# Optimization experiments

Hardware: AMD Instinct MI355X
Metric: run time of the kernel (lower is better)

Reference implementation:

```python
import jax, jax.numpy as jnp
import numpy as np

B, T, C, HS, E, NR, P = 2, 2048, 1024, 64, 8, 6, 4
H = C // HS
FF = 4 * C
NT = E - NR


def _ln(x, w, b):
    m = x.mean(-1, keepdims=True)
    v = x.var(-1, keepdims=True)
    return (x - m) * jax.lax.rsqrt(v + 1e-5) * w + b


def _rwkv_scan(r, k, v, w):
    # r,k,v,w: (B,T,H,D); per-head linear-attention recurrence with channel decay
    def step(S, inp):
        r_t, k_t, v_t, w_t = inp  # (B,H,D)
        S = S * w_t[..., :, None] + k_t[..., :, None] * v_t[..., None, :]
        y = jnp.einsum('bhk,bhkv->bhv', r_t, S)
        return S, y
    Bb, Tt, Hh, Dd = r.shape
    S0 = jnp.zeros((Bb, Hh, Dd, Dd), r.dtype)
    xs = tuple(jnp.moveaxis(a, 1, 0) for a in (r, k, v, w))
    _, ys = jax.lax.scan(step, S0, xs)
    return jnp.moveaxis(ys, 0, 1)


def setup_inputs() -> dict:
    key = jax.random.key(0)
    ks = jax.random.split(key, 24)
    s = 1.0 / np.sqrt(C)
    n = lambda k, sh, sc: jax.random.normal(k, sh, jnp.float32) * sc
    return {
        'x': n(ks[0], (B, T, C), 1.0),
        'v_first': jnp.zeros((B, T, C), jnp.float32),
        'capital_shares': jax.random.uniform(ks[1], (E,), dtype=jnp.float32),
        'ln1_w': jnp.ones((C,), jnp.float32), 'ln1_b': jnp.zeros((C,), jnp.float32),
        'ln2_w': jnp.ones((C,), jnp.float32), 'ln2_b': jnp.zeros((C,), jnp.float32),
        'Wr': n(ks[2], (C, C), s), 'Wk': n(ks[3], (C, C), s),
        'Wv': n(ks[4], (C, C), s), 'Ww': n(ks[5], (C, C), s),
        'w_bias': 2.0 * jnp.ones((C,), jnp.float32),
        'Wo': n(ks[6], (C, C), s),
        'conf_w': n(ks[7], (E, C), s), 'conf_b': jnp.zeros((E,), jnp.float32),
        'Wd': n(ks[8], (C, 1), s), 'bd': jnp.zeros((1,), jnp.float32),
        'Wa': n(ks[9], (C, E), s), 'ba': jnp.zeros((E,), jnp.float32),
        'Wb': n(ks[10], (2 * C, P * C), 1.0 / np.sqrt(2 * C)),
        'ffn_Wr': n(ks[11], (NR, C, C), s),
        'ffn_Wk': n(ks[12], (NR, C, FF), s),
        'ffn_Wv': n(ks[13], (NR, FF, C), 1.0 / np.sqrt(FF)),
        'tr_Wq': n(ks[14], (NT, C, C), s), 'tr_Wk': n(ks[15], (NT, C, C), s),
        'tr_Wv': n(ks[16], (NT, C, C), s), 'tr_Wo': n(ks[17], (NT, C, C), s),
    }


def _forward(x, v_first, capital_shares, ln1_w, ln1_b, ln2_w, ln2_b,
             Wr, Wk, Wv, Ww, w_bias, Wo, conf_w, conf_b, Wd, bd, Wa, ba, Wb,
             ffn_Wr, ffn_Wk, ffn_Wv, tr_Wq, tr_Wk, tr_Wv, tr_Wo):
    # --- attention stage: ln1 -> RWKV7 TimeMix -> residual -> ln2 ---
    x_ln = _ln(x, ln1_w, ln1_b)
    r = (x_ln @ Wr).reshape(B, T, H, HS)
    k = (x_ln @ Wk).reshape(B, T, H, HS)
    v_flat = x_ln @ Wv
    v = v_flat.reshape(B, T, H, HS)
    w = jax.nn.sigmoid(x_ln @ Ww + w_bias).reshape(B, T, H, HS)  # decay in (0,1)
    rwkv_state = _rwkv_scan(r, k, v, w).reshape(B, T, C)
    att_out = rwkv_state @ Wo
    x_after_att = x + att_out
    h = _ln(x_after_att, ln2_w, ln2_b)
    # --- no-grad market routing: confidences + critic + top-2 auction ---
    rh = jax.lax.stop_gradient(h)
    conf = jax.nn.sigmoid(jnp.einsum('btc,ec->bte', rh, conf_w) + conf_b)  # (B,T,E)
    difficulty = jax.nn.softplus(rh @ Wd + bd)          # (B,T,1)
    affinity = rh @ Wa + ba                             # (B,T,E)
    subsidy = jax.nn.softmax(affinity, axis=-1)         # critic subsidy
    bids = conf * capital_shares + subsidy
    top_vals, winners = jax.lax.top_k(bids, 2)          # (B,T,2)
    weights = jax.lax.stop_gradient(jax.nn.softmax(top_vals, axis=-1))
    # --- bridge prefix for transformer experts ---
    BT = B * T
    flat_h = h.reshape(BT, C)
    flat_state = rwkv_state.reshape(BT, C)
    prefix = jnp.tanh(jnp.concatenate([flat_h, flat_state], -1) @ Wb).reshape(BT, P, C)
    # --- top-2 expert mixing: gate==0 for unselected tokens (same math as masked dispatch) ---
    final_out = jnp.zeros_like(h)
    scale = 1.0 / np.sqrt(HS)
    for e in range(E):
        gate = (weights * (winners == e)).sum(-1)  # (B,T)
        if e < NR:  # sparse RWKV FFN expert: relu^2 channel-mix with receptance gate
            kk = jax.nn.relu(h @ ffn_Wk[e]) ** 2
            out_e = jax.nn.sigmoid(h @ ffn_Wr[e]) * (kk @ ffn_Wv[e])
        else:       # linear transformer expert: cross-attend token over its bridge prefix
            t = e - NR
            q = (flat_h @ tr_Wq[t]).reshape(BT, H, HS)
            kp = (prefix @ tr_Wk[t]).reshape(BT, P, H, HS)
            vp = (prefix @ tr_Wv[t]).reshape(BT, P, H, HS)
            a = jax.nn.softmax(jnp.einsum('nhd,nphd->nhp', q, kp) * scale, -1)
            out_e = (jnp.einsum('nhp,nphd->nhd', a, vp).reshape(BT, C) @ tr_Wo[t]).reshape(B, T, C)
        final_out = final_out + gate[..., None] * out_e
    x_out = x_after_att + final_out
    return x_out, v_flat  # layer 0: v_first is set to the value projection


def reference(x, v_first, capital_shares, ln1_w, ln1_b, ln2_w, ln2_b,
              Wr, Wk, Wv, Ww, w_bias, Wo, conf_w, conf_b, Wd, bd, Wa, ba, Wb,
              ffn_Wr, ffn_Wk, ffn_Wv, tr_Wq, tr_Wk, tr_Wv, tr_Wo):
    return _forward(x, v_first, capital_shares, ln1_w, ln1_b, ln2_w, ln2_b,
                    Wr, Wk, Wv, Ww, w_bias, Wo, conf_w, conf_b, Wd, bd, Wa, ba, Wb,
                    ffn_Wr, ffn_Wk, ffn_Wv, tr_Wq, tr_Wk, tr_Wv, tr_Wo)
```

## Files before the change

kernel.cpp:

```cpp
#include <hip/hip_runtime.h>
#include <hip/hip_bf16.h>
#include <math.h>

#define Bn   2
#define Tn   2048
#define Cdim 1024
#define HSn  64
#define En   8
#define NRn  6
#define Pn   4
#define Hn   16
#define FFn  4096
#define NTn  2
#define BTn  4096
#define CHL  128
#define NCH  16

typedef __attribute__((ext_vector_type(8))) short bfrag;
typedef __attribute__((ext_vector_type(4))) float f32x4;

__device__ __forceinline__ void gl_lds16(const void* g, void* l) {
    __builtin_amdgcn_global_load_lds(
        (const __attribute__((address_space(1))) unsigned int*)g,
        (__attribute__((address_space(3))) unsigned int*)l, 16, 0, 0);
}

__device__ __forceinline__ float sigm(float v) { return 1.f / (1.f + expf(-v)); }

__global__ __launch_bounds__(256) void ln_kernel(const float* __restrict__ x,
                                                 const float* __restrict__ w,
                                                 const float* __restrict__ b,
                                                 float* __restrict__ out_f,
                                                 __hip_bfloat16* __restrict__ out_hi,
                                                 __hip_bfloat16* __restrict__ out_lo) {
    int row = blockIdx.x;
    const float* xr = x + (size_t)row * Cdim;
    float s = 0.f, s2 = 0.f;
    for (int c = threadIdx.x; c < Cdim; c += 256) {
        float v = xr[c];
        s += v; s2 += v * v;
    }
    __shared__ float rs[256], rs2[256];
    rs[threadIdx.x] = s; rs2[threadIdx.x] = s2;
    __syncthreads();
    for (int st = 128; st > 0; st >>= 1) {
        if (threadIdx.x < st) {
            rs[threadIdx.x]  += rs[threadIdx.x + st];
            rs2[threadIdx.x] += rs2[threadIdx.x + st];
        }
        __syncthreads();
    }
    float mean = rs[0] / Cdim;
    float var  = rs2[0] / Cdim - mean * mean;
    float inv  = rsqrtf(var + 1e-5f);
    for (int c = threadIdx.x; c < Cdim; c += 256) {
        float v = (xr[c] - mean) * inv * w[c] + b[c];
        size_t idx = (size_t)row * Cdim + c;
        if (out_f) out_f[idx] = v;
        if (out_hi) {
            __hip_bfloat16 hi = __float2bfloat16(v);
            out_hi[idx] = hi;
            if (out_lo) out_lo[idx] = __float2bfloat16(v - __bfloat162float(hi));
        }
    }
}

__global__ __launch_bounds__(256) void convT_kernel(const float* __restrict__ W,
                                                    __hip_bfloat16* __restrict__ Wt,
                                                    int K, int N) {
    __shared__ float tile[32][33];
    int k0 = blockIdx.y * 32, n0 = blockIdx.x * 32;
    int tx = threadIdx.x, ty = threadIdx.y;
#pragma unroll
    for (int i = 0; i < 32; i += 8)
        tile[ty + i][tx] = W[(size_t)(k0 + ty + i) * N + n0 + tx];
    __syncthreads();
#pragma unroll
    for (int i = 0; i < 32; i += 8)
        Wt[(size_t)(n0 + ty + i) * K + k0 + tx] = __float2bfloat16(tile[tx][ty + i]);
}

__global__ __launch_bounds__(256) void convT_split_kernel(const float* __restrict__ W,
                                                          __hip_bfloat16* __restrict__ Wh,
                                                          __hip_bfloat16* __restrict__ Wl,
                                                          int K, int N) {
    __shared__ float tile[32][33];
    int k0 = blockIdx.y * 32, n0 = blockIdx.x * 32;
    int tx = threadIdx.x, ty = threadIdx.y;
#pragma unroll
    for (int i = 0; i < 32; i += 8)
        tile[ty + i][tx] = W[(size_t)(k0 + ty + i) * N + n0 + tx];
    __syncthreads();
#pragma unroll
    for (int i = 0; i < 32; i += 8) {
        float v = tile[tx][ty + i];
        __hip_bfloat16 hi = __float2bfloat16(v);
        size_t o = (size_t)(n0 + ty + i) * K + k0 + tx;
        Wh[o] = hi;
        Wl[o] = __float2bfloat16(v - __bfloat162float(hi));
    }
}

__global__ __launch_bounds__(256) void convT_split4_kernel(
    const float* __restrict__ W0, const float* __restrict__ W1,
    const float* __restrict__ W2, const float* __restrict__ W3,
    __hip_bfloat16* __restrict__ Wh, __hip_bfloat16* __restrict__ Wl) {
    int z = blockIdx.z;
    const float* W = (z == 0) ? W0 : (z == 1) ? W1 : (z == 2) ? W2 : W3;
    __hip_bfloat16* Whz = Wh + (size_t)z * Cdim * Cdim;
    __hip_bfloat16* Wlz = Wl + (size_t)z * Cdim * Cdim;
    __shared__ float tile[32][33];
    int k0 = blockIdx.y * 32, n0 = blockIdx.x * 32;
    int tx = threadIdx.x, ty = threadIdx.y;
#pragma unroll
    for (int i = 0; i < 32; i += 8)
        tile[ty + i][tx] = W[(size_t)(k0 + ty + i) * Cdim + n0 + tx];
    __syncthreads();
#pragma unroll
    for (int i = 0; i < 32; i += 8) {
        float v = tile[tx][ty + i];
        __hip_bfloat16 hi = __float2bfloat16(v);
        size_t o = (size_t)(n0 + ty + i) * Cdim + k0 + tx;
        Whz[o] = hi;
        Wlz[o] = __float2bfloat16(v - __bfloat162float(hi));
    }
}

__global__ __launch_bounds__(256) void convT_ffn_kernel(
    const float* __restrict__ Wr, const float* __restrict__ Wk,
    const float* __restrict__ Wv, __hip_bfloat16* __restrict__ dRK,
    __hip_bfloat16* __restrict__ dV) {
    int z = blockIdx.z;
    const float* src; __hip_bfloat16* dst; int srcLD, dstLD;
    if (z == 0) {
        src = Wr; dst = dRK; srcLD = 1024; dstLD = 1024;
    } else if (z < 5) {
        int s = z - 1;
        src = Wk + (size_t)s * 1024;
        dst = dRK + (size_t)(1024 + s * 1024) * 1024;
        srcLD = FFn; dstLD = 1024;
    } else {
        int s = z - 5;
        src = Wv + (size_t)s * 1024 * Cdim;
        dst = dV + (size_t)s * 1024;
        srcLD = Cdim; dstLD = FFn;
    }
    __shared__ float tile[32][33];
    int k0 = blockIdx.y * 32, n0 = blockIdx.x * 32;
    int tx = threadIdx.x, ty = threadIdx.y;
#pragma unroll
    for (int i = 0; i < 32; i += 8)
        tile[ty + i][tx] = src[(size_t)(k0 + ty + i) * srcLD + n0 + tx];
    __syncthreads();
#pragma unroll
    for (int i = 0; i < 32; i += 8)
        dst[(size_t)(n0 + ty + i) * dstLD + k0 + tx] = __float2bfloat16(tile[tx][ty + i]);
}

__global__ __launch_bounds__(256) void convT_tr_kernel(
    const float* __restrict__ W0, const float* __restrict__ W1,
    const float* __restrict__ W2, const float* __restrict__ W3,
    __hip_bfloat16* __restrict__ dst) {
    int z = blockIdx.z;
    const float* W = (z == 0) ? W0 : (z == 1) ? W1 : (z == 2) ? W2 : W3;
    __hip_bfloat16* Wt = dst + (size_t)z * Cdim * Cdim;
    __shared__ float tile[32][33];
    int k0 = blockIdx.y * 32, n0 = blockIdx.x * 32;
    int tx = threadIdx.x, ty = threadIdx.y;
#pragma unroll
    for (int i = 0; i < 32; i += 8)
        tile[ty + i][tx] = W[(size_t)(k0 + ty + i) * Cdim + n0 + tx];
    __syncthreads();
#pragma unroll
    for (int i = 0; i < 32; i += 8)
        Wt[(size_t)(n0 + ty + i) * Cdim + k0 + tx] = __float2bfloat16(tile[tx][ty + i]);
}

enum { EP3_QKVW = 0, EP3_ADD = 1 };

template <int EP>
__global__ __launch_bounds__(256) void bgemm3_kernel(
    const __hip_bfloat16* __restrict__ Ah, const __hip_bfloat16* __restrict__ Al,
    const __hip_bfloat16* __restrict__ Bh, const __hip_bfloat16* __restrict__ Bl,
    float* __restrict__ o0, float* __restrict__ o1,
    float* __restrict__ o2, float* __restrict__ o3,
    int M, int N, int K, const float* __restrict__ aux) {
    __shared__ __align__(16) __hip_bfloat16 Ahs[4096], Als[4096], Bhs[4096], Bls[4096];
    int tid = threadIdx.x;
    int m0 = blockIdx.y * 128, n0 = blockIdx.x * 128;
    int l = tid & 63, wv = tid >> 6;
    int wm = (wv >> 1) * 64, wn = (wv & 1) * 64;
    int lr = l & 15, lq = l >> 4;

    f32x4 acc[4][4];
#pragma unroll
    for (int i = 0; i < 4; i++)
#pragma unroll
        for (int j = 0; j < 4; j++) acc[i][j] = (f32x4){0.f, 0.f, 0.f, 0.f};

    int srow = tid >> 2;
    int sq = (tid & 3) ^ (srow & 3);
    size_t arow = (size_t)(m0 + srow) * K + (sq << 3);
    size_t brow = (size_t)(n0 + srow) * K + (sq << 3);

    for (int kt = 0; kt < K; kt += 32) {
#pragma unroll
        for (int r = 0; r < 2; r++) {
            size_t go = (size_t)(r * 64) * K + kt;
            int lo = r * 2048 + tid * 8;
            gl_lds16(Ah + arow + go, Ahs + lo);
            gl_lds16(Al + arow + go, Als + lo);
            gl_lds16(Bh + brow + go, Bhs + lo);
            gl_lds16(Bl + brow + go, Bls + lo);
        }
        __syncthreads();
        bfrag ah[4], al[4], bh[4], bl[4];
#pragma unroll
        for (int mi = 0; mi < 4; mi++) {
            int rr = wm + mi * 16 + lr;
            int off = rr * 32 + ((lq ^ (rr & 3)) << 3);
            ah[mi] = *(const bfrag*)&Ahs[off];
            al[mi] = *(const bfrag*)&Als[off];
        }
#pragma unroll
        for (int ni = 0; ni < 4; ni++) {
            int rr = wn + ni * 16 + lr;
            int off = rr * 32 + ((lq ^ (rr & 3)) << 3);
            bh[ni] = *(const bfrag*)&Bhs[off];
            bl[ni] = *(const bfrag*)&Bls[off];
        }
#pragma unroll
        for (int mi = 0; mi < 4; mi++)
#pragma unroll
            for (int ni = 0; ni < 4; ni++) {
                acc[mi][ni] = __builtin_amdgcn_mfma_f32_16x16x32_bf16(ah[mi], bh[ni], acc[mi][ni], 0, 0, 0);
                acc[mi][ni] = __builtin_amdgcn_mfma_f32_16x16x32_bf16(al[mi], bh[ni], acc[mi][ni], 0, 0, 0);
                acc[mi][ni] = __builtin_amdgcn_mfma_f32_16x16x32_bf16(ah[mi], bl[ni], acc[mi][ni], 0, 0, 0);
            }
        __syncthreads();
    }

#pragma unroll
    for (int mi = 0; mi < 4; mi++) {
#pragma unroll
        for (int r = 0; r < 4; r++) {
            int row = m0 + wm + mi * 16 + lq * 4 + r;
#pragma unroll
            for (int ni = 0; ni < 4; ni++) {
                int col = n0 + wn + ni * 16 + lr;
                float v = acc[mi][ni][r];
                if (EP == EP3_QKVW) {
                    int sel = col >> 10, cc = col & 1023;
                    size_t idx = (size_t)row * 1024 + cc;
                    if (sel == 0) o0[idx] = v;
                    else if (sel == 1) o1[idx] = v;
                    else if (sel == 2) o2[idx] = v;
                    else o3[idx] = sigm(v + aux[cc]);
                } else {
                    size_t idx = (size_t)row * N + col;
                    o0[idx] = aux[idx] + v;
                }
            }
        }
    }
}

enum { EP_TANHB = 0, EP_BF16 = 1, EP_MOE = 2, EP_MOEM = 3, EP_FFN1 = 4, EP_KV = 5 };

template <int EP>
__global__ __launch_bounds__(256) void bgemm_kernel(
    const __hip_bfloat16* __restrict__ A, const __hip_bfloat16* __restrict__ Bt,
    void* __restrict__ Cv, void* __restrict__ Cv2, int M, int N, int K,
    const int* __restrict__ meta, int e,
    const int* __restrict__ tokidx, const float* __restrict__ tokgate,
    const float* __restrict__ aux2) {
    int rows = M;
    int offA = 0;
    const int* sidx = nullptr;
    const float* sgate = nullptr;
    if (meta) {
        if (EP == EP_TANHB) {
            rows = meta[6] + meta[7];
        } else if (EP == EP_KV) {
            rows = meta[e] * 4;
            offA = (meta[8 + e] - meta[14]) * 4;
        } else {
            rows = meta[e];
            if (EP == EP_MOE || EP == EP_MOEM) {
                sidx = tokidx + meta[8 + e];
                sgate = tokgate + meta[8 + e];
            } else {
                offA = meta[8 + e];
            }
        }
    }
    int m0 = blockIdx.y * 128;
    if (m0 >= rows) return;

    __shared__ __align__(16) __hip_bfloat16 Asm[8192];
    __shared__ __align__(16) __hip_bfloat16 Bsm[8192];
    int tid = threadIdx.x;
    int n0 = blockIdx.x * 128;
    int l = tid & 63, wv = tid >> 6;
    int wm = (wv >> 1) * 64, wn = (wv & 1) * 64;
    int lr = l & 15, lq = l >> 4;

    f32x4 acc[4][4];
#pragma unroll
    for (int i = 0; i < 4; i++)
#pragma unroll
        for (int j = 0; j < 4; j++) acc[i][j] = (f32x4){0.f, 0.f, 0.f, 0.f};

    int srow = tid >> 3;
    int sq = (tid & 7) ^ (srow & 7);
    size_t arow = (size_t)(m0 + offA + srow) * K + (sq << 3);
    size_t brow = (size_t)(n0 + srow) * K + (sq << 3);

    int ks = K / gridDim.z;
    int kbeg = blockIdx.z * ks, kend = kbeg + ks;

    for (int kt = kbeg; kt < kend; kt += 64) {
#pragma unroll
        for (int c = 0; c < 4; c++) {
            size_t go = (size_t)(c * 32) * K + kt;
            gl_lds16(A + arow + go, Asm + c * 2048 + tid * 8);
            gl_lds16(Bt + brow + go, Bsm + c * 2048 + tid * 8);
        }
        __syncthreads();
#pragma unroll
        for (int kc = 0; kc < 64; kc += 32) {
            bfrag af[4], bf[4];
#pragma unroll
            for (int mi = 0; mi < 4; mi++) {
                int rr = wm + mi * 16 + lr;
                af[mi] = *(const bfrag*)&Asm[rr * 64 + ((((kc >> 3) + lq) ^ (rr & 7)) << 3)];
            }
#pragma unroll
            for (int ni = 0; ni < 4; ni++) {
                int rr = wn + ni * 16 + lr;
                bf[ni] = *(const bfrag*)&Bsm[rr * 64 + ((((kc >> 3) + lq) ^ (rr & 7)) << 3)];
            }
#pragma unroll
            for (int mi = 0; mi < 4; mi++)
#pragma unroll
                for (int ni = 0; ni < 4; ni++)
                    acc[mi][ni] = __builtin_amdgcn_mfma_f32_16x16x32_bf16(
                        af[mi], bf[ni], acc[mi][ni], 0, 0, 0);
        }
        __syncthreads();
    }

    float* Cf = (float*)Cv;
    __hip_bfloat16* Cb = (__hip_bfloat16*)Cv;
#pragma unroll
    for (int mi = 0; mi < 4; mi++) {
#pragma unroll
        for (int r = 0; r < 4; r++) {
            int row = m0 + wm + mi * 16 + lq * 4 + r;
            if (row >= rows) continue;
            int t = 0; float g = 0.f;
            if (EP == EP_MOE || EP == EP_MOEM) { t = sidx[row]; g = sgate[row]; }
#pragma unroll
            for (int ni = 0; ni < 4; ni++) {
                int col = n0 + wn + ni * 16 + lr;
                float v = acc[mi][ni][r];
                if (EP == EP_TANHB) {
                    Cb[(size_t)row * N + col] = __float2bfloat16(tanhf(v));
                } else if (EP == EP_BF16) {
                    Cb[(size_t)row * N + col] = __float2bfloat16(v);
                } else if (EP == EP_MOE) {
                    float* p = Cf + (size_t)t * 1024 + col;
                    *p = *p + g * v;
                } else if (EP == EP_MOEM) {
                    atomicAdd(Cf + (size_t)t * 1024 + col,
                              g * aux2[(size_t)row * 1024 + col] * v);
                } else if (EP == EP_FFN1) {
                    if ((col >> 10) == 0) {
                        Cf[(size_t)row * 1024 + col] = sigm(v);
                    } else {
                        float q = fmaxf(v, 0.f);
                        ((__hip_bfloat16*)Cv2)[(size_t)row * 4096 + col - 1024] =
                            __float2bfloat16(q * q);
                    }
                } else if (EP == EP_KV) {
                    if ((col >> 10) == 0)
                        Cb[(size_t)row * 1024 + col] = __float2bfloat16(v);
                    else
                        ((__hip_bfloat16*)Cv2)[(size_t)row * 1024 + col - 1024] =
                            __float2bfloat16(v);
                }
            }
        }
    }
}

__global__ __launch_bounds__(256) void scan_pass1(
    const float* __restrict__ k, const float* __restrict__ v,
    const float* __restrict__ w, float* __restrict__ Mbuf,
    float* __restrict__ Pbuf) {
    int c = blockIdx.x, bh = blockIdx.y;
    int b = bh >> 4, h = bh & 15;
    int tid = threadIdx.x, j = tid & 63, ig = tid >> 6;
    __shared__ float sbuf[2][3][64];
    float S[16], P[16];
#pragma unroll
    for (int ii = 0; ii < 16; ii++) { S[ii] = 0.f; P[ii] = 1.f; }

    size_t base = ((size_t)b * Tn + (size_t)c * CHL) * Cdim + (size_t)h * HSn + j;
    const float* srcs[3] = {k, v, w};
    const float* myp = (ig > 0) ? srcs[ig - 1] + base : k + base;

    const int CH = 8;
    float buf[CH];
#pragma unroll
    for (int u = 0; u < CH; u++) buf[u] = (ig > 0) ? myp[(size_t)u * Cdim] : 0.f;

    for (int tc = 0; tc < CHL; tc += CH) {
        float nbuf[CH];
#pragma unroll
        for (int u = 0; u < CH; u++) {
            int t2 = tc + CH + u;
            nbuf[u] = (ig > 0 && t2 < CHL) ? myp[(size_t)t2 * Cdim] : 0.f;
        }
#pragma unroll
        for (int u = 0; u < CH; u++) {
            int p = (tc + u) & 1;
            if (ig > 0) sbuf[p][ig - 1][j] = buf[u];
            __syncthreads();
            float vj = sbuf[p][1][j];
            const float* skp = sbuf[p][0];
            const float* swp = sbuf[p][2];
#pragma unroll
            for (int ii = 0; ii < 16; ii++) {
                int i = (ig << 4) + ii;
                float wi = swp[i];
                S[ii] = S[ii] * wi + skp[i] * vj;
                P[ii] *= wi;
            }
        }
#pragma unroll
        for (int u = 0; u < CH; u++) buf[u] = nbuf[u];
    }
    size_t mo = ((size_t)c * 32 + bh) * 4096;
#pragma unroll
    for (int ii = 0; ii < 16; ii++)
        Mbuf[mo + (size_t)((ig << 4) + ii) * 64 + j] = S[ii];
    if (j == 0) {
#pragma unroll
        for (int ii = 0; ii < 16; ii++)
            Pbuf[((size_t)c * 32 + bh) * 64 + (ig << 4) + ii] = P[ii];
    }
}

__global__ __launch_bounds__(256) void scan_pass2(
    const float* __restrict__ Mbuf, const float* __restrict__ Pbuf,
    float* __restrict__ Sinb) {
    int bh = blockIdx.y;
    int idx = blockIdx.x * 256 + threadIdx.x;
    int i = idx >> 6;
    float S = 0.f;
    for (int c = 0; c < NCH; c++) {
        size_t o = ((size_t)c * 32 + bh);
        Sinb[o * 4096 + idx] = S;
        S = Pbuf[o * 64 + i] * S + Mbuf[o * 4096 + idx];
    }
}

__global__ __launch_bounds__(256) void scan_pass3(
    const float* __restrict__ r, const float* __restrict__ k,
    const float* __restrict__ v, const float* __restrict__ w,
    const float* __restrict__ Sinb,
    __hip_bfloat16* __restrict__ sh, __hip_bfloat16* __restrict__ sl) {
    int c = blockIdx.x, bh = blockIdx.y;
    int b = bh >> 4, h = bh & 15;
    int tid = threadIdx.x, j = tid & 63, ig = tid >> 6;
    __shared__ float sbuf[2][4][64];
    __shared__ float red[2][4][64];
    float S[16];
    size_t so = ((size_t)c * 32 + bh) * 4096;
#pragma unroll
    for (int ii = 0; ii < 16; ii++)
        S[ii] = Sinb[so + (size_t)((ig << 4) + ii) * 64 + j];

    size_t base = ((size_t)b * Tn + (size_t)c * CHL) * Cdim + (size_t)h * HSn + j;
    const float* srcs[4] = {r, k, v, w};
    const float* myp = srcs[ig] + base;

    const int CH = 8;
    float buf[CH];
#pragma unroll
    for (int u = 0; u < CH; u++) buf[u] = myp[(size_t)u * Cdim];
    float part_prev = 0.f;

    for (int tc = 0; tc < CHL; tc += CH) {
        float nbuf[CH];
#pragma unroll
        for (int u = 0; u < CH; u++) {
            int t2 = tc + CH + u;
            nbuf[u] = (t2 < CHL) ? myp[(size_t)t2 * Cdim] : 0.f;
        }
#pragma unroll
        for (int u = 0; u < CH; u++) {
            int t = tc + u;
            int p = t & 1;
            sbuf[p][ig][j] = buf[u];
            red[p][ig][j] = part_prev;
            __syncthreads();
            if (ig == 0 && t > 0) {
                float val = red[p][0][j] + red[p][1][j] + red[p][2][j] + red[p][3][j];
                __hip_bfloat16 hi = __float2bfloat16(val);
                size_t pos = base + (size_t)(t - 1) * Cdim;
                sh[pos] = hi;
                sl[pos] = __float2bfloat16(val - __bfloat162float(hi));
            }
            float vj = sbuf[p][2][j];
            const float* srp = sbuf[p][0];
            const float* skp = sbuf[p][1];
            const float* swp = sbuf[p][3];
            float part = 0.f;
#pragma unroll
            for (int ii = 0; ii < 16; ii++) {
                int i = (ig << 4) + ii;
                S[ii] = S[ii] * swp[i] + skp[i] * vj;
                part += srp[i] * S[ii];
            }
            part_prev = part;
        }
#pragma unroll
        for (int u = 0; u < CH; u++) buf[u] = nbuf[u];
    }
    red[0][ig][j] = part_prev;
    __syncthreads();
    if (ig == 0) {
        float val = red[0][0][j] + red[0][1][j] + red[0][2][j] + red[0][3][j];
        __hip_bfloat16 hi = __float2bfloat16(val);
        size_t pos = base + (size_t)(CHL - 1) * Cdim;
        sh[pos] = hi;
        sl[pos] = __float2bfloat16(val - __bfloat162float(hi));
    }
}

__global__ __launch_bounds__(256) void routing_kernel(
    const float* __restrict__ h, const float* __restrict__ conf_w,
    const float* __restrict__ conf_b, const float* __restrict__ Wa,
    const float* __restrict__ ba, const float* __restrict__ cap,
    int* __restrict__ meta, int2* __restrict__ winfo, float2* __restrict__ gvals) {
    int row = blockIdx.x;
    const float* hr = h + (size_t)row * Cdim;
    float pc[8], pa[8];
#pragma unroll
    for (int e = 0; e < 8; e++) { pc[e] = 0.f; pa[e] = 0.f; }
    for (int c = threadIdx.x; c < Cdim; c += 256) {
        float hv = hr[c];
#pragma unroll
        for (int e = 0; e < 8; e++) {
            pc[e] += hv * conf_w[(size_t)e * Cdim + c];
            pa[e] += hv * Wa[(size_t)c * En + e];
        }
    }
    __shared__ float red[256];
    __shared__ float vals[16];
    for (int e = 0; e < 16; e++) {
        red[threadIdx.x] = (e < 8) ? pc[e] : pa[e - 8];
        __syncthreads();
        for (int st = 128; st > 0; st >>= 1) {
            if (threadIdx.x < st) red[threadIdx.x] += red[threadIdx.x + st];
            __syncthreads();
        }
        if (threadIdx.x == 0) vals[e] = red[0];
        __syncthreads();
    }
    if (threadIdx.x == 0) {
        float conf[8], aff[8];
        for (int e = 0; e < 8; e++) {
            conf[e] = sigm(vals[e] + conf_b[e]);
            aff[e]  = vals[8 + e] + ba[e];
        }
        float mx = aff[0];
        for (int e = 1; e < 8; e++) mx = fmaxf(mx, aff[e]);
        float se = 0.f, ex[8];
        for (int e = 0; e < 8; e++) { ex[e] = expf(aff[e] - mx); se += ex[e]; }
        float bids[8];
        for (int e = 0; e < 8; e++) bids[e] = conf[e] * cap[e] + ex[e] / se;
        int w0 = 0;
        for (int e = 1; e < 8; e++) if (bids[e] > bids[w0]) w0 = e;
        int w1 = -1;
        for (int e = 0; e < 8; e++) {
            if (e == w0) continue;
            if (w1 < 0 || bids[e] > bids[w1]) w1 = e;
        }
        float e1 = expf(bids[w1] - bids[w0]);
        float g0 = 1.f / (1.f + e1);
        float g1 = e1 / (1.f + e1);
        winfo[row] = make_int2(w0, w1);
        gvals[row] = make_float2(g0, g1);
        atomicAdd(&meta[w0], 1);
        atomicAdd(&meta[w1], 1);
    }
}

__global__ void offsets_kernel(int* __restrict__ meta) {
    if (threadIdx.x == 0 && blockIdx.x == 0) {
        int acc = 0;
        for (int e = 0; e < 8; e++) { meta[8 + e] = acc; acc += meta[e]; }
    }
}

__global__ __launch_bounds__(256) void assign_kernel(
    const int2* __restrict__ winfo, const float2* __restrict__ gvals,
    const int* __restrict__ meta, int* __restrict__ tokidx,
    float* __restrict__ tokgate, int2* __restrict__ posbuf) {
    int e = blockIdx.x;
    int tid = threadIdx.x;
    __shared__ int scn[256];
    int base = meta[8 + e];
    for (int c = 0; c < BTn; c += 256) {
        int t = c + tid;
        int2 w = winfo[t];
        int m0 = (w.x == e) ? 1 : 0;
        int m1 = (w.y == e) ? 1 : 0;
        int cnt = m0 + m1;
        scn[tid] = cnt;
        __syncthreads();
        for (int st = 1; st < 256; st <<= 1) {
            int vv = (tid >= st) ? scn[tid - st] : 0;
            __syncthreads();
            scn[tid] += vv;
            __syncthreads();
        }
        int excl = scn[tid] - cnt;
        int tot = scn[255];
        if (m0) {
            int p = base + excl;
            tokidx[p] = t; tokgate[p] = gvals[t].x; posbuf[t].x = p;
        }
        if (m1) {
            int p = base + excl;
            tokidx[p] = t; tokgate[p] = gvals[t].y; posbuf[t].y = p;
        }
        base += tot;
        __syncthreads();
    }
}

__global__ __launch_bounds__(256) void gather_kernel(
    const __hip_bfloat16* __restrict__ h_bf, const __hip_bfloat16* __restrict__ st,
    const int2* __restrict__ winfo, const int2* __restrict__ posbuf,
    const int* __restrict__ meta,
    __hip_bfloat16* __restrict__ hc, __hip_bfloat16* __restrict__ hsc) {
    int t = blockIdx.x;
    int tid = threadIdx.x;
    int2 w = winfo[t];
    int2 p = posbuf[t];
    int off6 = meta[14];
    ushort4 hv = ((const ushort4*)(h_bf + (size_t)t * 1024))[tid];
    ((ushort4*)(hc + (size_t)p.x * 1024))[tid] = hv;
    ((ushort4*)(hc + (size_t)p.y * 1024))[tid] = hv;
    if (w.x >= 6) {
        int lp = p.x - off6;
        ((ushort4*)(hsc + (size_t)lp * 2048))[tid] = hv;
        ((ushort4*)(hsc + (size_t)lp * 2048 + 1024))[tid] =
            ((const ushort4*)(st + (size_t)t * 1024))[tid];
    }
    if (w.y >= 6) {
        int lp = p.y - off6;
        ((ushort4*)(hsc + (size_t)lp * 2048))[tid] = hv;
        ((ushort4*)(hsc + (size_t)lp * 2048 + 1024))[tid] =
            ((const ushort4*)(st + (size_t)t * 1024))[tid];
    }
}

__global__ __launch_bounds__(256) void tr_attn_kernel(
    const __hip_bfloat16* __restrict__ qc, const __hip_bfloat16* __restrict__ kpc,
    const __hip_bfloat16* __restrict__ vpc, __hip_bfloat16* __restrict__ attnc,
    const int* __restrict__ meta, int e) {
    int cnt = meta[e];
    int idx = blockIdx.x * 4 + (threadIdx.x >> 6);
    int lane = threadIdx.x & 63;
    int n = idx >> 4, h = idx & 15;
    if (n >= cnt) return;
    float qd = __bfloat162float(qc[(size_t)n * Cdim + (size_t)h * HSn + lane]);
    float s[4];
#pragma unroll
    for (int p = 0; p < 4; p++) {
        float t = qd * __bfloat162float(kpc[((size_t)n * Pn + p) * Cdim + (size_t)h * HSn + lane]);
        for (int off = 32; off > 0; off >>= 1) t += __shfl_down(t, off);
        s[p] = __shfl(t, 0);
    }
    const float scale = 0.125f;
    float mx = fmaxf(fmaxf(s[0], s[1]), fmaxf(s[2], s[3])) * scale;
    float es = 0.f, a[4];
#pragma unroll
    for (int p = 0; p < 4; p++) { a[p] = expf(s[p] * scale - mx); es += a[p]; }
    float o = 0.f;
#pragma unroll
    for (int p = 0; p < 4; p++)
        o += (a[p] / es) * __bfloat162float(vpc[((size_t)n * Pn + p) * Cdim + (size_t)h * HSn + lane]);
    attnc[(size_t)n * Cdim + (size_t)h * HSn + lane] = __float2bfloat16(o);
}

extern "C" void kernel_launch(void* const* d_in, const int* in_sizes, int n_in,
                              void* d_out, int out_size, void* d_ws, size_t ws_size,
                              hipStream_t stream) {
    const float* x      = (const float*)d_in[0];
    const float* cap    = (const float*)d_in[2];
    const float* ln1_w  = (const float*)d_in[3];
    const float* ln1_b  = (const float*)d_in[4];
    const float* ln2_w  = (const float*)d_in[5];
    const float* ln2_b  = (const float*)d_in[6];
    const float* Wr     = (const float*)d_in[7];
    const float* Wk     = (const float*)d_in[8];
    const float* Wv     = (const float*)d_in[9];
    const float* Ww     = (const float*)d_in[10];
    const float* w_bias = (const float*)d_in[11];
    const float* Wo     = (const float*)d_in[12];
    const float* conf_w = (const float*)d_in[13];
    const float* conf_b = (const float*)d_in[14];
    const float* Wa     = (const float*)d_in[17];
    const float* ba     = (const float*)d_in[18];
    const float* Wb     = (const float*)d_in[19];
    const float* ffn_Wr = (const float*)d_in[20];
    const float* ffn_Wk = (const float*)d_in[21];
    const float* ffn_Wv = (const float*)d_in[22];
    const float* tr_Wq  = (const float*)d_in[23];
    const float* tr_Wk  = (const float*)d_in[24];
    const float* tr_Wv  = (const float*)d_in[25];
    const float* tr_Wo  = (const float*)d_in[26];

    float* xout  = (float*)d_out;
    float* vflat = (float*)d_out + (size_t)BTn * Cdim;

    char* ws = (char*)d_ws;
    const size_t MB = 1ull << 20;
    __hip_bfloat16* xln_hi  = (__hip_bfloat16*)(ws + 0 * MB);
    __hip_bfloat16* xln_lo  = (__hip_bfloat16*)(ws + 8 * MB);
    __hip_bfloat16* Wall_hi = (__hip_bfloat16*)(ws + 16 * MB);
    __hip_bfloat16* Wall_lo = (__hip_bfloat16*)(ws + 24 * MB);
    float*          rbuf    = (float*)(ws + 32 * MB);
    float*          kbuf    = (float*)(ws + 48 * MB);
    float*          wbuf    = (float*)(ws + 64 * MB);
    float*          Pbuf    = (float*)(ws + 80 * MB);
    __hip_bfloat16* Wo_hi   = (__hip_bfloat16*)(ws + 81 * MB);
    __hip_bfloat16* Wo_lo   = (__hip_bfloat16*)(ws + 83 * MB);
    float*          Mbuf    = (float*)(ws + 0 * MB);
    float*          Sinb    = (float*)(ws + 8 * MB);
    __hip_bfloat16* st_hi   = (__hip_bfloat16*)(ws + 16 * MB);
    __hip_bfloat16* st_lo   = (__hip_bfloat16*)(ws + 24 * MB);
    float*          hbuf    = (float*)(ws + 32 * MB);
    __hip_bfloat16* h_bf    = (__hip_bfloat16*)(ws + 48 * MB);
    __hip_bfloat16* hc      = (__hip_bfloat16*)(ws + 56 * MB);
    __hip_bfloat16* hsc     = (__hip_bfloat16*)(ws + 74 * MB);
    __hip_bfloat16* Wt_b    = (__hip_bfloat16*)(ws + 108 * MB);
    __hip_bfloat16* prefixc = (__hip_bfloat16*)(ws + 124 * MB);
    __hip_bfloat16* eWall   = (__hip_bfloat16*)(ws + 0 * MB);
    __hip_bfloat16* eWv_t   = (__hip_bfloat16*)(ws + 10 * MB);
    float*          rg      = (float*)(ws + 18 * MB);
    __hip_bfloat16* kk      = (__hip_bfloat16*)(ws + 74 * MB);
    __hip_bfloat16* vpc     = (__hip_bfloat16*)(ws + 0 * MB);
    __hip_bfloat16* tkv     = (__hip_bfloat16*)(ws + 34 * MB);
    __hip_bfloat16* tq      = (__hip_bfloat16*)(ws + 38 * MB);
    __hip_bfloat16* to_     = (__hip_bfloat16*)(ws + 40 * MB);
    __hip_bfloat16* qc      = (__hip_bfloat16*)(ws + 42 * MB);
    __hip_bfloat16* attnc   = (__hip_bfloat16*)(ws + 74 * MB);
    __hip_bfloat16* kpc     = (__hip_bfloat16*)(ws + 83 * MB);
    int*    meta    = (int*)(ws + 200 * MB);
    int*    tokidx  = (int*)(ws + 200 * MB + (64 << 10));
    float*  tokgate = (float*)(ws + 200 * MB + (128 << 10));
    int2*   winfo   = (int2*)(ws + 200 * MB + (192 << 10));
    float2* gvals   = (float2*)(ws + 200 * MB + (256 << 10));
    int2*   posbuf  = (int2*)(ws + 200 * MB + (320 << 10));
    (void)ws_size; (void)in_sizes; (void)n_in; (void)out_size;

    dim3 blk(256);
    dim3 tblk(32, 8);
    auto grid  = [](int M, int N) { return dim3(N / 128, M / 128); };
    auto tgrid = [](int K, int N) { return dim3(N / 32, K / 32); };
    const size_t CC = (size_t)Cdim * Cdim;

    hipMemsetAsync(meta, 0, 96, stream);
    convT_split4_kernel<<<dim3(32, 32, 4), tblk, 0, stream>>>(Wr, Wk, Wv, Ww, Wall_hi, Wall_lo);
    convT_split_kernel<<<tgrid(Cdim, Cdim), tblk, 0, stream>>>(Wo, Wo_hi, Wo_lo, Cdim, Cdim);
    convT_kernel<<<tgrid(2 * Cdim, Pn * Cdim), tblk, 0, stream>>>(Wb, Wt_b, 2 * Cdim, Pn * Cdim);

    ln_kernel<<<BTn, blk, 0, stream>>>(x, ln1_w, ln1_b, nullptr, xln_hi, xln_lo);
    bgemm3_kernel<EP3_QKVW><<<grid(BTn, 4 * Cdim), blk, 0, stream>>>(
        xln_hi, xln_lo, Wall_hi, Wall_lo, rbuf, kbuf, vflat, wbuf, BTn, 4 * Cdim, Cdim, w_bias);
    scan_pass1<<<dim3(NCH, 32), blk, 0, stream>>>(kbuf, vflat, wbuf, Mbuf, Pbuf);
    scan_pass2<<<dim3(16, 32), blk, 0, stream>>>(Mbuf, Pbuf, Sinb);
    scan_pass3<<<dim3(NCH, 32), blk, 0, stream>>>(rbuf, kbuf, vflat, wbuf, Sinb, st_hi, st_lo);
    bgemm3_kernel<EP3_ADD><<<grid(BTn, Cdim), blk, 0, stream>>>(
        st_hi, st_lo, Wo_hi, Wo_lo, xout, nullptr, nullptr, nullptr, BTn, Cdim, Cdim, x);
    ln_kernel<<<BTn, blk, 0, stream>>>(xout, ln2_w, ln2_b, hbuf, h_bf, nullptr);
    routing_kernel<<<BTn, blk, 0, stream>>>(hbuf, conf_w, conf_b, Wa, ba, cap, meta, winfo, gvals);
    offsets_kernel<<<1, 64, 0, stream>>>(meta);
    assign_kernel<<<dim3(8), blk, 0, stream>>>(winfo, gvals, meta, tokidx, tokgate, posbuf);
    gather_kernel<<<BTn, blk, 0, stream>>>(h_bf, st_hi, winfo, posbuf, meta, hc, hsc);
    bgemm_kernel<EP_TANHB><<<grid(2 * BTn, Pn * Cdim), blk, 0, stream>>>(
        hsc, Wt_b, prefixc, nullptr, 2 * BTn, Pn * Cdim, 2 * Cdim, meta, 0, nullptr, nullptr, nullptr);
    for (int e = 0; e < NRn; e++) {
        convT_ffn_kernel<<<dim3(32, 32, 9), tblk, 0, stream>>>(
            ffn_Wr + (size_t)e * CC, ffn_Wk + (size_t)e * Cdim * FFn,
            ffn_Wv + (size_t)e * FFn * Cdim, eWall, eWv_t);
        bgemm_kernel<EP_FFN1><<<grid(BTn, 5 * Cdim), blk, 0, stream>>>(
            hc, eWall, rg, kk, BTn, 5 * Cdim, Cdim, meta, e, nullptr, nullptr, nullptr);
        bgemm_kernel<EP_MOEM><<<dim3(Cdim / 128, BTn / 128, 2), blk, 0, stream>>>(
            kk, eWv_t, xout, nullptr, BTn, Cdim, FFn, meta, e, tokidx, tokgate, rg);
    }
    for (int t = 0; t < NTn; t++) {
        int e = NRn + t;
        convT_tr_kernel<<<dim3(32, 32, 4), tblk, 0, stream>>>(
            tr_Wk + (size_t)t * CC, tr_Wv + (size_t)t * CC,
            tr_Wq + (size_t)t * CC, tr_Wo + (size_t)t * CC, tkv);
        bgemm_kernel<EP_KV><<<grid(4 * BTn, 2 * Cdim), blk, 0, stream>>>(
            prefixc, tkv, kpc, vpc, 4 * BTn, 2 * Cdim, Cdim, meta, e, nullptr, nullptr, nullptr);
        bgemm_kernel<EP_BF16><<<grid(BTn, Cdim), blk, 0, stream>>>(
            hc, tq, qc, nullptr, BTn, Cdim, Cdim, meta, e, nullptr, nullptr, nullptr);
        tr_attn_kernel<<<(BTn * Hn) / 4, blk, 0, stream>>>(qc, kpc, vpc, attnc, meta, e);
        bgemm_kernel<EP_MOE><<<grid(BTn, Cdim), blk, 0, stream>>>(
            attnc, to_, xout, nullptr, BTn, Cdim, Cdim, meta, e, tokidx, tokgate, nullptr);
    }
}
```

Measured before the change: 1.760 ms.

## Fuse LN2 with routing, batch transformer experts, deepen bgemm3 K-tile

Merges the second layernorm with the routing kernel and removes the offsets kernel by computing expert prefix offsets inside assign_kernel. The two transformer experts' weight conversions, KV projections, Q projections and attention are each batched into a single launch using blockIdx.z. The split-bf16 bgemm3 kernel now loads 64-wide K tiles with an 8-way swizzle, which halves the barrier count and doubles its LDS use. The aim is to cut launch count, intermediate fp32 traffic and sync overhead, at the cost of more LDS per block and more workspace reshuffling.

```diff
diff --git a/kernel.cpp b/kernel.cpp
--- a/kernel.cpp
+++ b/kernel.cpp
@@ -62,6 +62,86 @@
             out_hi[idx] = hi;
             if (out_lo) out_lo[idx] = __float2bfloat16(v - __bfloat162float(hi));
         }
+    }
+}
+
+__global__ __launch_bounds__(256) void ln2_routing_kernel(
+    const float* __restrict__ x, const float* __restrict__ w,
+    const float* __restrict__ b, __hip_bfloat16* __restrict__ out_hi,
+    const float* __restrict__ conf_w, const float* __restrict__ conf_b,
+    const float* __restrict__ Wa, const float* __restrict__ ba,
+    const float* __restrict__ cap, int* __restrict__ meta,
+    int2* __restrict__ winfo, float2* __restrict__ gvals) {
+    int row = blockIdx.x;
+    const float* xr = x + (size_t)row * Cdim;
+    float s = 0.f, s2 = 0.f;
+    for (int c = threadIdx.x; c < Cdim; c += 256) {
+        float v = xr[c];
+        s += v; s2 += v * v;
+    }
+    __shared__ float rs[256], rs2[256];
+    rs[threadIdx.x] = s; rs2[threadIdx.x] = s2;
+    __syncthreads();
+    for (int st = 128; st > 0; st >>= 1) {
+        if (threadIdx.x < st) {
+            rs[threadIdx.x]  += rs[threadIdx.x + st];
+            rs2[threadIdx.x] += rs2[threadIdx.x + st];
+        }
+        __syncthreads();
+    }
+    float mean = rs[0] / Cdim;
+    float var  = rs2[0] / Cdim - mean * mean;
+    float inv  = rsqrtf(var + 1e-5f);
+    float pc[8], pa[8];
+#pragma unroll
+    for (int e = 0; e < 8; e++) { pc[e] = 0.f; pa[e] = 0.f; }
+    for (int c = threadIdx.x; c < Cdim; c += 256) {
+        float hv = (xr[c] - mean) * inv * w[c] + b[c];
+        out_hi[(size_t)row * Cdim + c] = __float2bfloat16(hv);
+#pragma unroll
+        for (int e = 0; e < 8; e++) {
+            pc[e] += hv * conf_w[(size_t)e * Cdim + c];
+            pa[e] += hv * Wa[(size_t)c * En + e];
+        }
+    }
+    __shared__ float red[256];
+    __shared__ float vals[16];
+    for (int e = 0; e < 16; e++) {
+        red[threadIdx.x] = (e < 8) ? pc[e] : pa[e - 8];
+        __syncthreads();
+        for (int st = 128; st > 0; st >>= 1) {
+            if (threadIdx.x < st) red[threadIdx.x] += red[threadIdx.x + st];
+            __syncthreads();
+        }
+        if (threadIdx.x == 0) vals[e] = red[0];
+        __syncthreads();
+    }
+    if (threadIdx.x == 0) {
+        float conf[8], aff[8];
+        for (int e = 0; e < 8; e++) {
+            conf[e] = sigm(vals[e] + conf_b[e]);
+            aff[e]  = vals[8 + e] + ba[e];
+        }
+        float mx = aff[0];
+        for (int e = 1; e < 8; e++) mx = fmaxf(mx, aff[e]);
+        float se = 0.f, ex[8];
+        for (int e = 0; e < 8; e++) { ex[e] = expf(aff[e] - mx); se += ex[e]; }
+        float bids[8];
+        for (int e = 0; e < 8; e++) bids[e] = conf[e] * cap[e] + ex[e] / se;
+        int w0 = 0;
+        for (int e = 1; e < 8; e++) if (bids[e] > bids[w0]) w0 = e;
+        int w1 = -1;
+        for (int e = 0; e < 8; e++) {
+            if (e == w0) continue;
+            if (w1 < 0 || bids[e] > bids[w1]) w1 = e;
+        }
+        float e1 = expf(bids[w1] - bids[w0]);
+        float g0 = 1.f / (1.f + e1);
+        float g1 = e1 / (1.f + e1);
+        winfo[row] = make_int2(w0, w1);
+        gvals[row] = make_float2(g0, g1);
+        atomicAdd(&meta[w0], 1);
+        atomicAdd(&meta[w1], 1);
     }
 }
 
@@ -157,12 +237,14 @@
         dst[(size_t)(n0 + ty + i) * dstLD + k0 + tx] = __float2bfloat16(tile[tx][ty + i]);
 }
 
-__global__ __launch_bounds__(256) void convT_tr_kernel(
-    const float* __restrict__ W0, const float* __restrict__ W1,
-    const float* __restrict__ W2, const float* __restrict__ W3,
+__global__ __launch_bounds__(256) void convT_tr8_kernel(
+    const float* __restrict__ Wk, const float* __restrict__ Wv,
+    const float* __restrict__ Wq, const float* __restrict__ Wo,
     __hip_bfloat16* __restrict__ dst) {
     int z = blockIdx.z;
-    const float* W = (z == 0) ? W0 : (z == 1) ? W1 : (z == 2) ? W2 : W3;
+    int t = z >> 2, j = z & 3;
+    const float* srcs[4] = {Wk, Wv, Wq, Wo};
+    const float* W = srcs[j] + (size_t)t * Cdim * Cdim;
     __hip_bfloat16* Wt = dst + (size_t)z * Cdim * Cdim;
     __shared__ float tile[32][33];
     int k0 = blockIdx.y * 32, n0 = blockIdx.x * 32;
@@ -175,6 +257,7 @@
     for (int i = 0; i < 32; i += 8)
         Wt[(size_t)(n0 + ty + i) * Cdim + k0 + tx] = __float2bfloat16(tile[tx][ty + i]);
 }
+
 
 enum { EP3_QKVW = 0, EP3_ADD = 1 };
 
@@ -185,7 +268,7 @@
     float* __restrict__ o0, float* __restrict__ o1,
     float* __restrict__ o2, float* __restrict__ o3,
     int M, int N, int K, const float* __restrict__ aux) {
-    __shared__ __align__(16) __hip_bfloat16 Ahs[4096], Als[4096], Bhs[4096], Bls[4096];
+    __shared__ __align__(16) __hip_bfloat16 Ahs[8192], Als[8192], Bhs[8192], Bls[8192];
     int tid = threadIdx.x;
     int m0 = blockIdx.y * 128, n0 = blockIdx.x * 128;
     int l = tid & 63, wv = tid >> 6;
@@ -198,45 +281,47 @@
 #pragma unroll
         for (int j = 0; j < 4; j++) acc[i][j] = (f32x4){0.f, 0.f, 0.f, 0.f};
 
-    int srow = tid >> 2;
-    int sq = (tid & 3) ^ (srow & 3);
+    int srow = tid >> 3;
+    int sq = (tid & 7) ^ (srow & 7);
     size_t arow = (size_t)(m0 + srow) * K + (sq << 3);
     size_t brow = (size_t)(n0 + srow) * K + (sq << 3);
 
-    for (int kt = 0; kt < K; kt += 32) {
-#pragma unroll
-        for (int r = 0; r < 2; r++) {
-            size_t go = (size_t)(r * 64) * K + kt;
-            int lo = r * 2048 + tid * 8;
-            gl_lds16(Ah + arow + go, Ahs + lo);
-            gl_lds16(Al + arow + go, Als + lo);
-            gl_lds16(Bh + brow + go, Bhs + lo);
-            gl_lds16(Bl + brow + go, Bls + lo);
-        }
-        __syncthreads();
-        bfrag ah[4], al[4], bh[4], bl[4];
-#pragma unroll
-        for (int mi = 0; mi < 4; mi++) {
-            int rr = wm + mi * 16 + lr;
-            int off = rr * 32 + ((lq ^ (rr & 3)) << 3);
-            ah[mi] = *(const bfrag*)&Ahs[off];
-            al[mi] = *(const bfrag*)&Als[off];
-        }
-#pragma unroll
-        for (int ni = 0; ni < 4; ni++) {
-            int rr = wn + ni * 16 + lr;
-            int off = rr * 32 + ((lq ^ (rr & 3)) << 3);
-            bh[ni] = *(const bfrag*)&Bhs[off];
-            bl[ni] = *(const bfrag*)&Bls[off];
-        }
-#pragma unroll
-        for (int mi = 0; mi < 4; mi++)
+    for (int kt = 0; kt < K; kt += 64) {
+#pragma unroll
+        for (int c = 0; c < 4; c++) {
+            size_t go = (size_t)(c * 32) * K + kt;
+            gl_lds16(Ah + arow + go, Ahs + c * 2048 + tid * 8);
+            gl_lds16(Al + arow + go, Als + c * 2048 + tid * 8);
+            gl_lds16(Bh + brow + go, Bhs + c * 2048 + tid * 8);
+            gl_lds16(Bl + brow + go, Bls + c * 2048 + tid * 8);
+        }
+        __syncthreads();
+#pragma unroll
+        for (int kc = 0; kc < 64; kc += 32) {
+            bfrag ah[4], al[4], bh[4], bl[4];
+#pragma unroll
+            for (int mi = 0; mi < 4; mi++) {
+                int rr = wm + mi * 16 + lr;
+                int off = rr * 64 + ((((kc >> 3) + lq) ^ (rr & 7)) << 3);
+                ah[mi] = *(const bfrag*)&Ahs[off];
+                al[mi] = *(const bfrag*)&Als[off];
+            }
 #pragma unroll
             for (int ni = 0; ni < 4; ni++) {
-                acc[mi][ni] = __builtin_amdgcn_mfma_f32_16x16x32_bf16(ah[mi], bh[ni], acc[mi][ni], 0, 0, 0);
-                acc[mi][ni] = __builtin_amdgcn_mfma_f32_16x16x32_bf16(al[mi], bh[ni], acc[mi][ni], 0, 0, 0);
-                acc[mi][ni] = __builtin_amdgcn_mfma_f32_16x16x32_bf16(ah[mi], bl[ni], acc[mi][ni], 0, 0, 0);
+                int rr = wn + ni * 16 + lr;
+                int off = rr * 64 + ((((kc >> 3) + lq) ^ (rr & 7)) << 3);
+                bh[ni] = *(const bfrag*)&Bhs[off];
+                bl[ni] = *(const bfrag*)&Bls[off];
             }
+#pragma unroll
+            for (int mi = 0; mi < 4; mi++)
+#pragma unroll
+                for (int ni = 0; ni < 4; ni++) {
+                    acc[mi][ni] = __builtin_amdgcn_mfma_f32_16x16x32_bf16(ah[mi], bh[ni], acc[mi][ni], 0, 0, 0);
+                    acc[mi][ni] = __builtin_amdgcn_mfma_f32_16x16x32_bf16(al[mi], bh[ni], acc[mi][ni], 0, 0, 0);
+                    acc[mi][ni] = __builtin_amdgcn_mfma_f32_16x16x32_bf16(ah[mi], bl[ni], acc[mi][ni], 0, 0, 0);
+                }
+        }
         __syncthreads();
     }
 
@@ -265,7 +350,7 @@
     }
 }
 
-enum { EP_TANHB = 0, EP_BF16 = 1, EP_MOE = 2, EP_MOEM = 3, EP_FFN1 = 4, EP_KV = 5 };
+enum { EP_TANHB = 0, EP_Q = 1, EP_MOE = 2, EP_MOEM = 3, EP_FFN1 = 4, EP_KV = 5 };
 
 template <int EP>
 __global__ __launch_bounds__(256) void bgemm_kernel(
@@ -274,24 +359,40 @@
     const int* __restrict__ meta, int e,
     const int* __restrict__ tokidx, const float* __restrict__ tokgate,
     const float* __restrict__ aux2) {
+    const size_t CC_ = (size_t)Cdim * Cdim;
     int rows = M;
     int offA = 0;
+    int outoff = 0;
+    const __hip_bfloat16* Bp = Bt;
     const int* sidx = nullptr;
     const float* sgate = nullptr;
     if (meta) {
         if (EP == EP_TANHB) {
             rows = meta[6] + meta[7];
         } else if (EP == EP_KV) {
-            rows = meta[e] * 4;
-            offA = (meta[8 + e] - meta[14]) * 4;
+            int zx = blockIdx.z;
+            rows = meta[6 + zx] * 4;
+            offA = (meta[8 + 6 + zx] - meta[14]) * 4;
+            outoff = offA;
+            Bp = Bt + (size_t)(zx * 4) * CC_;
+        } else if (EP == EP_Q) {
+            int zx = blockIdx.z;
+            rows = meta[6 + zx];
+            offA = meta[8 + 6 + zx];
+            outoff = meta[8 + 6 + zx] - meta[14];
+            Bp = Bt + (size_t)(zx * 4 + 2) * CC_;
+        } else if (EP == EP_MOE) {
+            rows = meta[e];
+            offA = meta[8 + e] - meta[14];
+            sidx = tokidx + meta[8 + e];
+            sgate = tokgate + meta[8 + e];
+        } else if (EP == EP_MOEM) {
+            rows = meta[e];
+            sidx = tokidx + meta[8 + e];
+            sgate = tokgate + meta[8 + e];
         } else {
             rows = meta[e];
-            if (EP == EP_MOE || EP == EP_MOEM) {
-                sidx = tokidx + meta[8 + e];
-                sgate = tokgate + meta[8 + e];
-            } else {
-                offA = meta[8 + e];
-            }
+            offA = meta[8 + e];
         }
     }
     int m0 = blockIdx.y * 128;
@@ -316,15 +417,20 @@
     size_t arow = (size_t)(m0 + offA + srow) * K + (sq << 3);
     size_t brow = (size_t)(n0 + srow) * K + (sq << 3);
 
-    int ks = K / gridDim.z;
-    int kbeg = blockIdx.z * ks, kend = kbeg + ks;
+    int kbeg, kend;
+    if (EP == EP_KV || EP == EP_Q) {
+        kbeg = 0; kend = K;
+    } else {
+        int ks = K / gridDim.z;
+        kbeg = blockIdx.z * ks; kend = kbeg + ks;
+    }
 
     for (int kt = kbeg; kt < kend; kt += 64) {
 #pragma unroll
         for (int c = 0; c < 4; c++) {
             size_t go = (size_t)(c * 32) * K + kt;
             gl_lds16(A + arow + go, Asm + c * 2048 + tid * 8);
-            gl_lds16(Bt + brow + go, Bsm + c * 2048 + tid * 8);
+            gl_lds16(Bp + brow + go, Bsm + c * 2048 + tid * 8);
         }
         __syncthreads();
 #pragma unroll
@@ -358,6 +464,7 @@
         for (int r = 0; r < 4; r++) {
             int row = m0 + wm + mi * 16 + lq * 4 + r;
             if (row >= rows) continue;
+            int orow = row + outoff;
             int t = 0; float g = 0.f;
             if (EP == EP_MOE || EP == EP_MOEM) { t = sidx[row]; g = sgate[row]; }
 #pragma unroll
@@ -366,8 +473,8 @@
                 float v = acc[mi][ni][r];
                 if (EP == EP_TANHB) {
                     Cb[(size_t)row * N + col] = __float2bfloat16(tanhf(v));
-                } else if (EP == EP_BF16) {
-                    Cb[(size_t)row * N + col] = __float2bfloat16(v);
+                } else if (EP == EP_Q) {
+                    Cb[(size_t)orow * N + col] = __float2bfloat16(v);
                 } else if (EP == EP_MOE) {
                     float* p = Cf + (size_t)t * 1024 + col;
                     *p = *p + g * v;
@@ -384,9 +491,9 @@
                     }
                 } else if (EP == EP_KV) {
                     if ((col >> 10) == 0)
-                        Cb[(size_t)row * 1024 + col] = __float2bfloat16(v);
+                        Cb[(size_t)orow * 1024 + col] = __float2bfloat16(v);
                     else
-                        ((__hip_bfloat16*)Cv2)[(size_t)row * 1024 + col - 1024] =
+                        ((__hip_bfloat16*)Cv2)[(size_t)orow * 1024 + col - 1024] =
                             __float2bfloat16(v);
                 }
             }
@@ -540,80 +647,16 @@
     }
 }
 
-__global__ __launch_bounds__(256) void routing_kernel(
-    const float* __restrict__ h, const float* __restrict__ conf_w,
-    const float* __restrict__ conf_b, const float* __restrict__ Wa,
-    const float* __restrict__ ba, const float* __restrict__ cap,
-    int* __restrict__ meta, int2* __restrict__ winfo, float2* __restrict__ gvals) {
-    int row = blockIdx.x;
-    const float* hr = h + (size_t)row * Cdim;
-    float pc[8], pa[8];
-#pragma unroll
-    for (int e = 0; e < 8; e++) { pc[e] = 0.f; pa[e] = 0.f; }
-    for (int c = threadIdx.x; c < Cdim; c += 256) {
-        float hv = hr[c];
-#pragma unroll
-        for (int e = 0; e < 8; e++) {
-            pc[e] += hv * conf_w[(size_t)e * Cdim + c];
-            pa[e] += hv * Wa[(size_t)c * En + e];
-        }
-    }
-    __shared__ float red[256];
-    __shared__ float vals[16];
-    for (int e = 0; e < 16; e++) {
-        red[threadIdx.x] = (e < 8) ? pc[e] : pa[e - 8];
-        __syncthreads();
-        for (int st = 128; st > 0; st >>= 1) {
-            if (threadIdx.x < st) red[threadIdx.x] += red[threadIdx.x + st];
-            __syncthreads();
-        }
-        if (threadIdx.x == 0) vals[e] = red[0];
-        __syncthreads();
-    }
-    if (threadIdx.x == 0) {
-        float conf[8], aff[8];
-        for (int e = 0; e < 8; e++) {
-            conf[e] = sigm(vals[e] + conf_b[e]);
-            aff[e]  = vals[8 + e] + ba[e];
-        }
-        float mx = aff[0];
-        for (int e = 1; e < 8; e++) mx = fmaxf(mx, aff[e]);
-        float se = 0.f, ex[8];
-        for (int e = 0; e < 8; e++) { ex[e] = expf(aff[e] - mx); se += ex[e]; }
-        float bids[8];
-        for (int e = 0; e < 8; e++) bids[e] = conf[e] * cap[e] + ex[e] / se;
-        int w0 = 0;
-        for (int e = 1; e < 8; e++) if (bids[e] > bids[w0]) w0 = e;
-        int w1 = -1;
-        for (int e = 0; e < 8; e++) {
-            if (e == w0) continue;
-            if (w1 < 0 || bids[e] > bids[w1]) w1 = e;
-        }
-        float e1 = expf(bids[w1] - bids[w0]);
-        float g0 = 1.f / (1.f + e1);
-        float g1 = e1 / (1.f + e1);
-        winfo[row] = make_int2(w0, w1);
-        gvals[row] = make_float2(g0, g1);
-        atomicAdd(&meta[w0], 1);
-        atomicAdd(&meta[w1], 1);
-    }
-}
-
-__global__ void offsets_kernel(int* __restrict__ meta) {
-    if (threadIdx.x == 0 && blockIdx.x == 0) {
-        int acc = 0;
-        for (int e = 0; e < 8; e++) { meta[8 + e] = acc; acc += meta[e]; }
-    }
-}
-
 __global__ __launch_bounds__(256) void assign_kernel(
     const int2* __restrict__ winfo, const float2* __restrict__ gvals,
-    const int* __restrict__ meta, int* __restrict__ tokidx,
+    int* __restrict__ meta, int* __restrict__ tokidx,
     float* __restrict__ tokgate, int2* __restrict__ posbuf) {
     int e = blockIdx.x;
     int tid = threadIdx.x;
     __shared__ int scn[256];
-    int base = meta[8 + e];
+    int base = 0;
+    for (int e2 = 0; e2 < e; ++e2) base += meta[e2];
+    if (tid == 0) meta[8 + e] = base;
     for (int c = 0; c < BTn; c += 256) {
         int t = c + tid;
         int2 w = winfo[t];
@@ -673,8 +716,8 @@
 __global__ __launch_bounds__(256) void tr_attn_kernel(
     const __hip_bfloat16* __restrict__ qc, const __hip_bfloat16* __restrict__ kpc,
     const __hip_bfloat16* __restrict__ vpc, __hip_bfloat16* __restrict__ attnc,
-    const int* __restrict__ meta, int e) {
-    int cnt = meta[e];
+    const int* __restrict__ meta) {
+    int cnt = meta[6] + meta[7];
     int idx = blockIdx.x * 4 + (threadIdx.x >> 6);
     int lane = threadIdx.x & 63;
     int n = idx >> 4, h = idx & 15;
@@ -746,7 +789,6 @@
     float*          Sinb    = (float*)(ws + 8 * MB);
     __hip_bfloat16* st_hi   = (__hip_bfloat16*)(ws + 16 * MB);
     __hip_bfloat16* st_lo   = (__hip_bfloat16*)(ws + 24 * MB);
-    float*          hbuf    = (float*)(ws + 32 * MB);
     __hip_bfloat16* h_bf    = (__hip_bfloat16*)(ws + 48 * MB);
     __hip_bfloat16* hc      = (__hip_bfloat16*)(ws + 56 * MB);
     __hip_bfloat16* hsc     = (__hip_bfloat16*)(ws + 74 * MB);
@@ -758,11 +800,9 @@
     __hip_bfloat16* kk      = (__hip_bfloat16*)(ws + 74 * MB);
     __hip_bfloat16* vpc     = (__hip_bfloat16*)(ws + 0 * MB);
     __hip_bfloat16* tkv     = (__hip_bfloat16*)(ws + 34 * MB);
-    __hip_bfloat16* tq      = (__hip_bfloat16*)(ws + 38 * MB);
-    __hip_bfloat16* to_     = (__hip_bfloat16*)(ws + 40 * MB);
-    __hip_bfloat16* qc      = (__hip_bfloat16*)(ws + 42 * MB);
-    __hip_bfloat16* attnc   = (__hip_bfloat16*)(ws + 74 * MB);
-    __hip_bfloat16* kpc     = (__hip_bfloat16*)(ws + 83 * MB);
+    __hip_bfloat16* kpc     = (__hip_bfloat16*)(ws + 74 * MB);
+    __hip_bfloat16* qc      = (__hip_bfloat16*)(ws + 108 * MB);
+    __hip_bfloat16* attnc   = (__hip_bfloat16*)(ws + 192 * MB);
     int*    meta    = (int*)(ws + 200 * MB);
     int*    tokidx  = (int*)(ws + 200 * MB + (64 << 10));
     float*  tokgate = (float*)(ws + 200 * MB + (128 << 10));
@@ -790,9 +830,8 @@
     scan_pass3<<<dim3(NCH, 32), blk, 0, stream>>>(rbuf, kbuf, vflat, wbuf, Sinb, st_hi, st_lo);
     bgemm3_kernel<EP3_ADD><<<grid(BTn, Cdim), blk, 0, stream>>>(
         st_hi, st_lo, Wo_hi, Wo_lo, xout, nullptr, nullptr, nullptr, BTn, Cdim, Cdim, x);
-    ln_kernel<<<BTn, blk, 0, stream>>>(xout, ln2_w, ln2_b, hbuf, h_bf, nullptr);
-    routing_kernel<<<BTn, blk, 0, stream>>>(hbuf, conf_w, conf_b, Wa, ba, cap, meta, winfo, gvals);
-    offsets_kernel<<<1, 64, 0, stream>>>(meta);
+    ln2_routing_kernel<<<BTn, blk, 0, stream>>>(
+        xout, ln2_w, ln2_b, h_bf, conf_w, conf_b, Wa, ba, cap, meta, winfo, gvals);
     assign_kernel<<<dim3(8), blk, 0, stream>>>(winfo, gvals, meta, tokidx, tokgate, posbuf);
     gather_kernel<<<BTn, blk, 0, stream>>>(h_bf, st_hi, winfo, posbuf, meta, hc, hsc);
     bgemm_kernel<EP_TANHB><<<grid(2 * BTn, Pn * Cdim), blk, 0, stream>>>(
@@ -806,17 +845,15 @@
         bgemm_kernel<EP_MOEM><<<dim3(Cdim / 128, BTn / 128, 2), blk, 0, stream>>>(
             kk, eWv_t, xout, nullptr, BTn, Cdim, FFn, meta, e, tokidx, tokgate, rg);
     }
+    convT_tr8_kernel<<<dim3(32, 32, 8), tblk, 0, stream>>>(tr_Wk, tr_Wv, tr_Wq, tr_Wo, tkv);
+    bgemm_kernel<EP_KV><<<dim3(16, 128, 2), blk, 0, stream>>>(
+        prefixc, tkv, kpc, vpc, 4 * BTn, 2 * Cdim, Cdim, meta, 6, nullptr, nullptr, nullptr);
+    bgemm_kernel<EP_Q><<<dim3(8, 32, 2), blk, 0, stream>>>(
+        hc, tkv, qc, nullptr, BTn, Cdim, Cdim, meta, 6, nullptr, nullptr, nullptr);
+    tr_attn_kernel<<<(BTn * Hn) / 4, blk, 0, stream>>>(qc, kpc, vpc, attnc, meta);
     for (int t = 0; t < NTn; t++) {
-        int e = NRn + t;
-        convT_tr_kernel<<<dim3(32, 32, 4), tblk, 0, stream>>>(
-            tr_Wk + (size_t)t * CC, tr_Wv + (size_t)t * CC,
-            tr_Wq + (size_t)t * CC, tr_Wo + (size_t)t * CC, tkv);
-        bgemm_kernel<EP_KV><<<grid(4 * BTn, 2 * Cdim), blk, 0, stream>>>(
-            prefixc, tkv, kpc, vpc, 4 * BTn, 2 * Cdim, Cdim, meta, e, nullptr, nullptr, nullptr);
-        bgemm_kernel<EP_BF16><<<grid(BTn, Cdim), blk, 0, stream>>>(
-            hc, tq, qc, nullptr, BTn, Cdim, Cdim, meta, e, nullptr, nullptr, nullptr);
-        tr_attn_kernel<<<(BTn * Hn) / 4, blk, 0, stream>>>(qc, kpc, vpc, attnc, meta, e);
         bgemm_kernel<EP_MOE><<<grid(BTn, Cdim), blk, 0, stream>>>(
-            attnc, to_, xout, nullptr, BTn, Cdim, Cdim, meta, e, tokidx, tokgate, nullptr);
-    }
-}
+            attnc, tkv + (size_t)(4 * t + 3) * CC, xout, nullptr,
+            BTn, Cdim, Cdim, meta, 6 + t, tokidx, tokgate, nullptr);
+    }
+}
```

New measurement: 1.885 ms. 1.07x slower.
